# Optimization experiments

Measured on AMD Instinct MI355X. Metric: run time of the kernel, lower is better.

## Reference

```python
import jax, jax.numpy as jnp
import numpy as np

SPATIAL_SHAPES = [(116, 200), (58, 100), (29, 50), (15, 25)]  # (H, W) per level
NUM_HEADS = 8
NUM_LEVELS = 4
NUM_POINTS = 8
NUM_Z = 4  # num_Z_anchors; NUM_POINTS must be divisible by NUM_Z
EMBED = 256


def _msda3d_forward(query, value, reference_points, w_off, b_off, w_attn, b_attn, w_val, b_val):
    bs, nq, _ = query.shape
    d = EMBED // NUM_HEADS
    # value projection -> (bs, num_value, heads, d)
    v = (value @ w_val + b_val).reshape(bs, -1, NUM_HEADS, d)
    # sampling offsets and attention weights from query
    off = (query @ w_off + b_off).reshape(bs, nq, NUM_HEADS, NUM_LEVELS, NUM_POINTS, 2)
    attn = (query @ w_attn + b_attn).reshape(bs, nq, NUM_HEADS, NUM_LEVELS * NUM_POINTS)
    attn = jax.nn.softmax(attn, axis=-1).reshape(bs, nq, NUM_HEADS, NUM_LEVELS, NUM_POINTS)
    # normalize offsets by (W, H) per level
    shapes = jnp.asarray(SPATIAL_SHAPES, dtype=query.dtype)  # (L,2) = (h,w)
    norm = jnp.stack([shapes[:, 1], shapes[:, 0]], axis=-1)  # (L,2) = (w,h)
    off = off / norm[None, None, None, :, None, :]
    # reference_points (bs,nq,Z,2) broadcast against offsets split over Z anchors
    p_per_z = NUM_POINTS // NUM_Z
    off = off.reshape(bs, nq, NUM_HEADS, NUM_LEVELS, p_per_z, NUM_Z, 2)
    loc = reference_points[:, :, None, None, None, :, :] + off
    loc = loc.reshape(bs, nq, NUM_HEADS, NUM_LEVELS, NUM_POINTS, 2)
    # per-level bilinear sampling (grid_sample, align_corners=False, zeros padding)
    out = jnp.zeros((bs, nq, NUM_HEADS, d), dtype=query.dtype)
    start = 0
    for lvl, (H, W) in enumerate(SPATIAL_SHAPES):
        v_l = v[:, start:start + H * W]  # (bs, H*W, heads, d)
        start += H * W
        locs = loc[:, :, :, lvl]  # (bs, nq, heads, P, 2) in [0,1]
        # grid = 2*loc-1, then unnormalize with align_corners=False: x = loc*W - 0.5
        x = locs[..., 0] * W - 0.5
        y = locs[..., 1] * H - 0.5
        x0 = jnp.floor(x)
        y0 = jnp.floor(y)
        lx = x - x0
        ly = y - y0
        x0i = x0.astype(jnp.int32)
        y0i = y0.astype(jnp.int32)
        samp = jnp.zeros((bs, nq, NUM_HEADS, NUM_POINTS, d), dtype=query.dtype)
        corners = ((0, 0, (1 - ly) * (1 - lx)), (0, 1, (1 - ly) * lx),
                   (1, 0, ly * (1 - lx)), (1, 1, ly * lx))
        for dy, dx, w in corners:
            xi = x0i + dx
            yi = y0i + dy
            valid = (xi >= 0) & (xi < W) & (yi >= 0) & (yi < H)
            idx = jnp.clip(yi, 0, H - 1) * W + jnp.clip(xi, 0, W - 1)  # (bs,nq,heads,P)
            # gather along flattened HW per (batch, head)
            idx2 = idx.transpose(0, 1, 3, 2).reshape(bs, nq * NUM_POINTS, NUM_HEADS)
            g = jnp.take_along_axis(v_l, idx2[..., None], axis=1)  # (bs, nq*P, heads, d)
            g = g.reshape(bs, nq, NUM_POINTS, NUM_HEADS, d).transpose(0, 1, 3, 2, 4)
            samp = samp + g * (w * valid.astype(query.dtype))[..., None]
        out = out + (samp * attn[:, :, :, lvl, :, None]).sum(axis=3)
    return out.reshape(bs, nq, EMBED)


def setup_inputs() -> dict:
    key = jax.random.key(0)
    ks = jax.random.split(key, 9)
    bs, nq = 6, 10000
    num_value = sum(h * w for h, w in SPATIAL_SHAPES)  # 30825
    return {
        "query": jax.random.normal(ks[0], (bs, nq, EMBED), jnp.float32),
        "value": jax.random.normal(ks[1], (bs, num_value, EMBED), jnp.float32),
        "reference_points": jax.random.uniform(ks[2], (bs, nq, NUM_Z, 2), jnp.float32),
        "w_off": jax.random.normal(ks[3], (EMBED, NUM_HEADS * NUM_LEVELS * NUM_POINTS * 2), jnp.float32) * 0.01,
        "b_off": jax.random.normal(ks[4], (NUM_HEADS * NUM_LEVELS * NUM_POINTS * 2,), jnp.float32) * 0.02,
        "w_attn": jax.random.normal(ks[5], (EMBED, NUM_HEADS * NUM_LEVELS * NUM_POINTS), jnp.float32) * 0.02,
        "b_attn": jnp.zeros((NUM_HEADS * NUM_LEVELS * NUM_POINTS,), jnp.float32),
        "w_val": jax.random.normal(ks[6], (EMBED, EMBED), jnp.float32) * 0.02,
        "b_val": jnp.zeros((EMBED,), jnp.float32),
    }


def reference(query, value, reference_points, w_off, b_off, w_attn, b_attn, w_val, b_val):
    return _msda3d_forward(query, value, reference_points, w_off, b_off, w_attn, b_attn, w_val, b_val)
```

## Files before the change

### kernel.cpp

```cpp
#include <hip/hip_runtime.h>
#include <hip/hip_bf16.h>

#define NQ 10000
#define BS 6
#define NV 30825

typedef __attribute__((ext_vector_type(8))) short bf16x8;
typedef __attribute__((ext_vector_type(4))) float f32x4;
typedef __attribute__((ext_vector_type(2))) float f32x2;

__device__ __forceinline__ void gload_lds16(const void* g, void* l) {
  __builtin_amdgcn_global_load_lds(
      (const __attribute__((address_space(1))) unsigned int*)g,
      (__attribute__((address_space(3))) unsigned int*)l, 16, 0, 0);
}

__device__ __forceinline__ unsigned short bf_bits(float f) {
  __hip_bfloat16 h = __float2bfloat16(f);
  return *(unsigned short*)&h;
}

__global__ __launch_bounds__(256) void f32_to_bf16_kernel(
    const float* __restrict__ in, unsigned short* __restrict__ out, int n4) {
  int i = blockIdx.x * 256 + threadIdx.x;
  if (i >= n4) return;
  float4 v = ((const float4*)in)[i];
  ushort4 o;
  o.x = bf_bits(v.x); o.y = bf_bits(v.y); o.z = bf_bits(v.z); o.w = bf_bits(v.w);
  ((ushort4*)out)[i] = o;
}

__global__ __launch_bounds__(256) void prep_weights_kernel(
    const float* __restrict__ w_val, const float* __restrict__ w_off,
    const float* __restrict__ w_attn, const float* __restrict__ b_off,
    const float* __restrict__ b_attn, unsigned short* __restrict__ wvalT,
    unsigned short* __restrict__ wpackT, float* __restrict__ bpack) {
  int i = blockIdx.x * 256 + threadIdx.x;
  if (i < 65536) {
    int n = i >> 8, k = i & 255;
    wvalT[i] = bf_bits(w_val[k * 256 + n]);
  } else if (i < 65536 + 196608) {
    int j = i - 65536;
    int n = j >> 8, k = j & 255;
    float v = (n < 512) ? w_off[k * 512 + n] : w_attn[k * 256 + (n - 512)];
    wpackT[j] = bf_bits(v);
  } else if (i < 65536 + 196608 + 768) {
    int j = i - 262144;
    bpack[j] = (j < 512) ? b_off[j] : b_attn[j - 512];
  }
}

__global__ __launch_bounds__(256) void gemm_mfma_kernel(
    const unsigned short* __restrict__ A, const unsigned short* __restrict__ WT,
    const float* __restrict__ bias, unsigned short* __restrict__ C, int M, int N) {
  __shared__ short As[128 * 64];
  __shared__ short Bs[128 * 64];
  const int tid = threadIdx.x;
  const int wv = tid >> 6;
  const int lane = tid & 63;
  const int wr = wv >> 1, wc = wv & 1;
  const int m0 = blockIdx.x * 128;
  const int n0 = blockIdx.y * 128;

  f32x4 acc[4][4] = {};

  for (int kt = 0; kt < 4; ++kt) {
#pragma unroll
    for (int j = 0; j < 4; ++j) {
      int u = j * 256 + tid;
      int row = u >> 3;
      int kbyte = (u & 7) * 16;
      int ldsoff = (j * 256 + wv * 64) * 16;
      int gr = m0 + row; if (gr >= M) gr = M - 1;
      gload_lds16((const char*)A + (size_t)gr * 512 + kt * 128 + kbyte,
                  (char*)As + ldsoff);
      gload_lds16((const char*)WT + (size_t)(n0 + row) * 512 + kt * 128 + kbyte,
                  (char*)Bs + ldsoff);
    }
    __syncthreads();
#pragma unroll
    for (int kk = 0; kk < 2; ++kk) {
      bf16x8 af[4], bfr[4];
#pragma unroll
      for (int mi = 0; mi < 4; ++mi) {
        int off = (wr * 64 + mi * 16 + (lane & 15)) * 64 + kk * 32 + (lane >> 4) * 8;
        af[mi] = *(const bf16x8*)&As[off];
      }
#pragma unroll
      for (int ni = 0; ni < 4; ++ni) {
        int off = (wc * 64 + ni * 16 + (lane & 15)) * 64 + kk * 32 + (lane >> 4) * 8;
        bfr[ni] = *(const bf16x8*)&Bs[off];
      }
#pragma unroll
      for (int mi = 0; mi < 4; ++mi)
#pragma unroll
        for (int ni = 0; ni < 4; ++ni)
          acc[mi][ni] = __builtin_amdgcn_mfma_f32_16x16x32_bf16(
              af[mi], bfr[ni], acc[mi][ni], 0, 0, 0);
    }
    __syncthreads();
  }

  const int colb = n0 + wc * 64 + (lane & 15);
  float bvn[4];
#pragma unroll
  for (int ni = 0; ni < 4; ++ni) bvn[ni] = bias[colb + ni * 16];
#pragma unroll
  for (int mi = 0; mi < 4; ++mi) {
#pragma unroll
    for (int r = 0; r < 4; ++r) {
      int row = m0 + wr * 64 + mi * 16 + (lane >> 4) * 4 + r;
      if (row < M) {
#pragma unroll
        for (int ni = 0; ni < 4; ++ni)
          C[(size_t)row * N + colb + ni * 16] = bf_bits(acc[mi][ni][r] + bvn[ni]);
      }
    }
  }
}

__global__ __launch_bounds__(256) void msda_sample_kernel(
    const __hip_bfloat16* __restrict__ vproj,
    const __hip_bfloat16* __restrict__ C2,
    const float* __restrict__ ref,
    float* __restrict__ out) {
  const int bq = blockIdx.x;
  const int b = bq / NQ;
  const int tid = threadIdx.x;

  __shared__ int4 s_iw4[2][271];

  {
    const int lp = tid & 31;
    const int l = lp >> 3, p = lp & 7, z = p & 3;
    const __hip_bfloat162* offp = (const __hip_bfloat162*)(C2 + (size_t)bq * 768);
    __hip_bfloat162 ob = offp[tid];
    float ox = __bfloat162float(ob.x), oy = __bfloat162float(ob.y);
    float logit = __bfloat162float(C2[(size_t)bq * 768 + 512 + tid]);

    float mx = logit;
#pragma unroll
    for (int m = 16; m >= 1; m >>= 1) mx = fmaxf(mx, __shfl_xor(mx, m, 32));
    float e = __expf(logit - mx);
    float s = e;
#pragma unroll
    for (int m = 16; m >= 1; m >>= 1) s += __shfl_xor(s, m, 32);
    float aw = e / s;

    float2 rz = *(const float2*)(ref + (size_t)bq * 8 + z * 2);
    const int W = 200 >> l;
    const int H = (l == 3) ? 15 : (116 >> l);
    const int base = (l == 0) ? 0 : (l == 1) ? 23200 : (l == 2) ? 29000 : 30450;

    float x = rz.x * (float)W + ox - 0.5f;
    float y = rz.y * (float)H + oy - 0.5f;
    float x0f = floorf(x), y0f = floorf(y);
    float lx = x - x0f, ly = y - y0f;
    int x0 = (int)x0f, y0 = (int)y0f;
    int x1 = x0 + 1, y1 = y0 + 1;

    float w00 = (1.f - ly) * (1.f - lx) * aw;
    float w01 = (1.f - ly) * lx * aw;
    float w10 = ly * (1.f - lx) * aw;
    float w11 = ly * lx * aw;

    if (!((x0 >= 0) & (x0 < W))) { w00 = 0.f; w10 = 0.f; }
    if (!((x1 >= 0) & (x1 < W))) { w01 = 0.f; w11 = 0.f; }
    if (!((y0 >= 0) & (y0 < H))) { w00 = 0.f; w01 = 0.f; }
    if (!((y1 >= 0) & (y1 < H))) { w10 = 0.f; w11 = 0.f; }

    int x0c = min(max(x0, 0), W - 1);
    int x1c = min(max(x1, 0), W - 1);
    int y0c = min(max(y0, 0), H - 1);
    int y1c = min(max(y1, 0), H - 1);

    int rb00 = (base + y0c * W + x0c) << 9;
    int rb01 = (base + y0c * W + x1c) << 9;
    int rb10 = (base + y1c * W + x0c) << 9;
    int rb11 = (base + y1c * W + x1c) << 9;

    const int it = tid + (tid >> 4);
    s_iw4[0][it] = make_int4(rb00, __float_as_int(w00), rb01, __float_as_int(w01));
    s_iw4[1][it] = make_int4(rb10, __float_as_int(w10), rb11, __float_as_int(w11));
  }
  __syncthreads();

  const int h = tid >> 5;
  const int half = (tid >> 4) & 1;
  const int lane16 = tid & 15;
  const unsigned laneoff = (unsigned)(h * 64 + lane16 * 4);
  const char* ubase = (const char*)vproj + (size_t)b * NV * 512;
  const int sbase = h * 32 + half * 16;
  const int sb2 = sbase + (sbase >> 4);

  f32x2 acc = {0.f, 0.f};
#pragma unroll 4
  for (int s = 0; s < 16; ++s) {
    int4 cA = s_iw4[0][sb2 + s];
    int4 cB = s_iw4[1][sb2 + s];
    unsigned v0 = *(const unsigned*)(ubase + (unsigned)(cA.x) + laneoff);
    unsigned v1 = *(const unsigned*)(ubase + (unsigned)(cA.z) + laneoff);
    unsigned v2 = *(const unsigned*)(ubase + (unsigned)(cB.x) + laneoff);
    unsigned v3 = *(const unsigned*)(ubase + (unsigned)(cB.z) + laneoff);
    f32x2 p0 = {__uint_as_float(v0 << 16), __uint_as_float(v0 & 0xffff0000u)};
    f32x2 p1 = {__uint_as_float(v1 << 16), __uint_as_float(v1 & 0xffff0000u)};
    f32x2 p2 = {__uint_as_float(v2 << 16), __uint_as_float(v2 & 0xffff0000u)};
    f32x2 p3 = {__uint_as_float(v3 << 16), __uint_as_float(v3 & 0xffff0000u)};
    acc += p0 * __int_as_float(cA.y);
    acc += p1 * __int_as_float(cA.w);
    acc += p2 * __int_as_float(cB.y);
    acc += p3 * __int_as_float(cB.w);
  }

  acc.x += __shfl_xor(acc.x, 16);
  acc.y += __shfl_xor(acc.y, 16);
  if (!half) {
    *(float2*)(out + (size_t)bq * 256 + h * 32 + lane16 * 2) =
        make_float2(acc.x, acc.y);
  }
}

extern "C" void kernel_launch(void* const* d_in, const int* in_sizes, int n_in,
                              void* d_out, int out_size, void* d_ws, size_t ws_size,
                              hipStream_t stream) {
  const float* query  = (const float*)d_in[0];
  const float* value  = (const float*)d_in[1];
  const float* refp   = (const float*)d_in[2];
  const float* w_off  = (const float*)d_in[3];
  const float* b_off  = (const float*)d_in[4];
  const float* w_attn = (const float*)d_in[5];
  const float* b_attn = (const float*)d_in[6];
  const float* w_val  = (const float*)d_in[7];
  const float* b_val  = (const float*)d_in[8];
  float* out = (float*)d_out;

  char* ws = (char*)d_ws;
  unsigned short* vproj  = (unsigned short*)(ws);
  unsigned short* valb   = (unsigned short*)(ws + 94694400);
  unsigned short* C2     = (unsigned short*)(ws + 94694400);
  unsigned short* qb     = (unsigned short*)(ws + 189388800);
  unsigned short* wvalT  = (unsigned short*)(ws + 220108800);
  unsigned short* wpackT = (unsigned short*)(ws + 220239872);
  float*          bpack  = (float*)        (ws + 220633088);

  const int Mv = BS * NV;
  const int Mq = BS * NQ;

  prep_weights_kernel<<<1032, 256, 0, stream>>>(w_val, w_off, w_attn, b_off, b_attn,
                                                wvalT, wpackT, bpack);
  f32_to_bf16_kernel<<<(Mv * 64 + 255) / 256, 256, 0, stream>>>(value, valb, Mv * 64);
  f32_to_bf16_kernel<<<(Mq * 64 + 255) / 256, 256, 0, stream>>>(query, qb, Mq * 64);
  gemm_mfma_kernel<<<dim3((Mv + 127) / 128, 2), 256, 0, stream>>>(
      valb, wvalT, b_val, vproj, Mv, 256);
  gemm_mfma_kernel<<<dim3((Mq + 127) / 128, 6), 256, 0, stream>>>(
      qb, wpackT, bpack, C2, Mq, 768);
  msda_sample_kernel<<<BS * NQ, 256, 0, stream>>>(
      (const __hip_bfloat16*)vproj, (const __hip_bfloat16*)C2, refp, out);
}
```

Baseline: 395.5 us.

## Fuse fp32-to-bf16 conversion into GEMM, widen N tile, double-buffer weights

Removes the two standalone fp32-to-bf16 conversion kernels. The GEMM now reads fp32 activations directly, converts them in registers and writes them to LDS. The GEMM block grows to 512 threads covering 128x256 output tiles, with double-buffered weight tiles and prefetch of the next K slice, so A is read once per row block instead of once per N tile. This cuts a full round-trip of the value and query tensors through memory and reduces redundant A loads. The cost is extra barriers per K step and more LDS per block, which may lower occupancy.

```diff
diff --git a/kernel.cpp b/kernel.cpp
--- a/kernel.cpp
+++ b/kernel.cpp
@@ -6,6 +6,7 @@
 #define NV 30825
 
 typedef __attribute__((ext_vector_type(8))) short bf16x8;
+typedef __attribute__((ext_vector_type(8))) unsigned short u16x8;
 typedef __attribute__((ext_vector_type(4))) float f32x4;
 typedef __attribute__((ext_vector_type(2))) float f32x2;
 
@@ -18,16 +19,6 @@
 __device__ __forceinline__ unsigned short bf_bits(float f) {
   __hip_bfloat16 h = __float2bfloat16(f);
   return *(unsigned short*)&h;
-}
-
-__global__ __launch_bounds__(256) void f32_to_bf16_kernel(
-    const float* __restrict__ in, unsigned short* __restrict__ out, int n4) {
-  int i = blockIdx.x * 256 + threadIdx.x;
-  if (i >= n4) return;
-  float4 v = ((const float4*)in)[i];
-  ushort4 o;
-  o.x = bf_bits(v.x); o.y = bf_bits(v.y); o.z = bf_bits(v.z); o.w = bf_bits(v.w);
-  ((ushort4*)out)[i] = o;
 }
 
 __global__ __launch_bounds__(256) void prep_weights_kernel(
@@ -50,34 +41,55 @@
   }
 }
 
-__global__ __launch_bounds__(256) void gemm_mfma_kernel(
-    const unsigned short* __restrict__ A, const unsigned short* __restrict__ WT,
+__global__ __launch_bounds__(512) void gemm_fused_kernel(
+    const float* __restrict__ A, const unsigned short* __restrict__ WT,
     const float* __restrict__ bias, unsigned short* __restrict__ C, int M, int N) {
   __shared__ short As[128 * 64];
-  __shared__ short Bs[128 * 64];
+  __shared__ short Bs[2][256 * 64];
   const int tid = threadIdx.x;
   const int wv = tid >> 6;
   const int lane = tid & 63;
-  const int wr = wv >> 1, wc = wv & 1;
+  const int wr = wv >> 2, wc = wv & 3;
   const int m0 = blockIdx.x * 128;
-  const int n0 = blockIdx.y * 128;
-
+  const int n0 = blockIdx.y * 256;
+
+  const int arow = tid >> 2, aq = tid & 3;
   f32x4 acc[4][4] = {};
-
-  for (int kt = 0; kt < 4; ++kt) {
+  float4 ar0, ar1, ar2, ar3;
+
+  auto loadA = [&](int kt) {
+    int gr = m0 + arow; if (gr >= M) gr = M - 1;
+    const float4* ap = (const float4*)(A + (size_t)gr * 256 + kt * 64 + aq * 16);
+    ar0 = ap[0]; ar1 = ap[1]; ar2 = ap[2]; ar3 = ap[3];
+  };
+  auto writeA = [&]() {
+    u16x8 p0 = { bf_bits(ar0.x), bf_bits(ar0.y), bf_bits(ar0.z), bf_bits(ar0.w),
+                 bf_bits(ar1.x), bf_bits(ar1.y), bf_bits(ar1.z), bf_bits(ar1.w) };
+    u16x8 p1 = { bf_bits(ar2.x), bf_bits(ar2.y), bf_bits(ar2.z), bf_bits(ar2.w),
+                 bf_bits(ar3.x), bf_bits(ar3.y), bf_bits(ar3.z), bf_bits(ar3.w) };
+    *(u16x8*)&As[arow * 64 + aq * 16] = p0;
+    *(u16x8*)&As[arow * 64 + aq * 16 + 8] = p1;
+  };
+  auto stageB = [&](int kt, int buf) {
 #pragma unroll
     for (int j = 0; j < 4; ++j) {
-      int u = j * 256 + tid;
+      int u = j * 512 + tid;
       int row = u >> 3;
       int kbyte = (u & 7) * 16;
-      int ldsoff = (j * 256 + wv * 64) * 16;
-      int gr = m0 + row; if (gr >= M) gr = M - 1;
-      gload_lds16((const char*)A + (size_t)gr * 512 + kt * 128 + kbyte,
-                  (char*)As + ldsoff);
+      int ldsoff = (j * 512 + wv * 64) * 16;
       gload_lds16((const char*)WT + (size_t)(n0 + row) * 512 + kt * 128 + kbyte,
-                  (char*)Bs + ldsoff);
-    }
-    __syncthreads();
+                  (char*)Bs[buf] + ldsoff);
+    }
+  };
+
+  loadA(0);
+  stageB(0, 0);
+  writeA();
+  __syncthreads();
+
+  for (int kt = 0; kt < 4; ++kt) {
+    if (kt < 3) { loadA(kt + 1); stageB(kt + 1, (kt + 1) & 1); }
+    const short* bs = Bs[kt & 1];
 #pragma unroll
     for (int kk = 0; kk < 2; ++kk) {
       bf16x8 af[4], bfr[4];
@@ -89,7 +101,7 @@
 #pragma unroll
       for (int ni = 0; ni < 4; ++ni) {
         int off = (wc * 64 + ni * 16 + (lane & 15)) * 64 + kk * 32 + (lane >> 4) * 8;
-        bfr[ni] = *(const bf16x8*)&Bs[off];
+        bfr[ni] = *(const bf16x8*)&bs[off];
       }
 #pragma unroll
       for (int mi = 0; mi < 4; ++mi)
@@ -98,7 +110,11 @@
           acc[mi][ni] = __builtin_amdgcn_mfma_f32_16x16x32_bf16(
               af[mi], bfr[ni], acc[mi][ni], 0, 0, 0);
     }
-    __syncthreads();
+    if (kt < 3) {
+      __syncthreads();
+      writeA();
+      __syncthreads();
+    }
   }
 
   const int colb = n0 + wc * 64 + (lane & 15);
@@ -236,24 +252,20 @@
 
   char* ws = (char*)d_ws;
   unsigned short* vproj  = (unsigned short*)(ws);
-  unsigned short* valb   = (unsigned short*)(ws + 94694400);
   unsigned short* C2     = (unsigned short*)(ws + 94694400);
-  unsigned short* qb     = (unsigned short*)(ws + 189388800);
-  unsigned short* wvalT  = (unsigned short*)(ws + 220108800);
-  unsigned short* wpackT = (unsigned short*)(ws + 220239872);
-  float*          bpack  = (float*)        (ws + 220633088);
+  unsigned short* wvalT  = (unsigned short*)(ws + 186854400);
+  unsigned short* wpackT = (unsigned short*)(ws + 186985472);
+  float*          bpack  = (float*)        (ws + 187378688);
 
   const int Mv = BS * NV;
   const int Mq = BS * NQ;
 
   prep_weights_kernel<<<1032, 256, 0, stream>>>(w_val, w_off, w_attn, b_off, b_attn,
                                                 wvalT, wpackT, bpack);
-  f32_to_bf16_kernel<<<(Mv * 64 + 255) / 256, 256, 0, stream>>>(value, valb, Mv * 64);
-  f32_to_bf16_kernel<<<(Mq * 64 + 255) / 256, 256, 0, stream>>>(query, qb, Mq * 64);
-  gemm_mfma_kernel<<<dim3((Mv + 127) / 128, 2), 256, 0, stream>>>(
-      valb, wvalT, b_val, vproj, Mv, 256);
-  gemm_mfma_kernel<<<dim3((Mq + 127) / 128, 6), 256, 0, stream>>>(
-      qb, wpackT, bpack, C2, Mq, 768);
+  gemm_fused_kernel<<<dim3((Mv + 127) / 128, 1), 512, 0, stream>>>(
+      value, wvalT, b_val, vproj, Mv, 256);
+  gemm_fused_kernel<<<dim3((Mq + 127) / 128, 3), 512, 0, stream>>>(
+      query, wpackT, bpack, C2, Mq, 768);
   msda_sample_kernel<<<BS * NQ, 256, 0, stream>>>(
       (const __hip_bfloat16*)vproj, (const __hip_bfloat16*)C2, refp, out);
 }
```

Result: faster. 377.1 us (-4.7%).
